# Kernel optimization log

Hardware: AMD Instinct MI355X
Metric: run time of the kernel (lower is better)

Reference implementation:

```python
import jax, jax.numpy as jnp
import numpy as np

D = 128
N_DRUG = 100000
N_PROT = 50000
E_DD, E_DP, E_PD = 800000, 600000, 600000
EPS = 1e-5


def setup_inputs() -> dict:
    key = jax.random.key(0)
    ks = jax.random.split(key, 19)
    f32 = jnp.float32
    return {
        "x_drug": jax.random.normal(ks[0], (N_DRUG, D), f32),
        "x_prot": jax.random.normal(ks[1], (N_PROT, D), f32),
        "Wagg_dd": jax.random.normal(ks[2], (D, D), f32) * 0.05,
        "Wagg_dp": jax.random.normal(ks[3], (D, D), f32) * 0.05,
        "Wagg_pd": jax.random.normal(ks[4], (D, D), f32) * 0.05,
        "W_drug": jax.random.normal(ks[5], (D, 2 * D), f32) * 0.05,
        "b_drug": jax.random.normal(ks[6], (D,), f32) * 0.01,
        "W_prot": jax.random.normal(ks[7], (D, 2 * D), f32) * 0.05,
        "b_prot": jax.random.normal(ks[8], (D,), f32) * 0.01,
        "g_drug": jnp.ones((D,), f32),
        "be_drug": jnp.zeros((D,), f32),
        "g_prot": jnp.ones((D,), f32),
        "be_prot": jnp.zeros((D,), f32),
        "ei_dd_src": jax.random.randint(ks[9], (E_DD,), 0, N_DRUG, jnp.int64 if jax.config.jax_enable_x64 else jnp.int32),
        "ei_dd_dst": jax.random.randint(ks[10], (E_DD,), 0, N_DRUG),
        "ei_dp_src": jax.random.randint(ks[11], (E_DP,), 0, N_DRUG),
        "ei_dp_dst": jax.random.randint(ks[12], (E_DP,), 0, N_PROT),
        "ei_pd_src": jax.random.randint(ks[13], (E_PD,), 0, N_PROT),
        "ei_pd_dst": jax.random.randint(ks[14], (E_PD,), 0, N_DRUG),
    }


def _rel_agg(x_src, W_agg, src_idx, dst_idx, n_dst):
    # gather -> per-relation Linear (no bias) + ReLU -> scatter-mean
    h = jax.nn.relu(x_src[src_idx] @ W_agg.T)            # [E, D]
    s = jax.ops.segment_sum(h, dst_idx, num_segments=n_dst)
    c = jax.ops.segment_sum(jnp.ones((src_idx.shape[0],), h.dtype), dst_idx, num_segments=n_dst)
    return s / jnp.maximum(c, 1.0)[:, None]


def _layernorm(x, g, b):
    mu = jnp.mean(x, axis=-1, keepdims=True)
    var = jnp.mean(jnp.square(x - mu), axis=-1, keepdims=True)
    return (x - mu) * jax.lax.rsqrt(var + EPS) * g + b


def _node_update(h_self, h_agg, W, b, g, be):
    h = jax.nn.relu(jnp.concatenate([h_self, h_agg], axis=-1) @ W.T + b)
    return _layernorm(h + h_self, g, be)  # dropout is identity in eval


def reference(x_drug, x_prot, Wagg_dd, Wagg_dp, Wagg_pd, W_drug, b_drug,
              W_prot, b_prot, g_drug, be_drug, g_prot, be_prot,
              ei_dd_src, ei_dd_dst, ei_dp_src, ei_dp_dst, ei_pd_src, ei_pd_dst):
    agg_dd = _rel_agg(x_drug, Wagg_dd, ei_dd_src, ei_dd_dst, N_DRUG)
    agg_pd = _rel_agg(x_prot, Wagg_pd, ei_pd_src, ei_pd_dst, N_DRUG)
    agg_drug = (agg_dd + agg_pd) * 0.5                   # mean over relations into 'drug'
    agg_prot = _rel_agg(x_drug, Wagg_dp, ei_dp_src, ei_dp_dst, N_PROT)
    out_drug = _node_update(x_drug, agg_drug, W_drug, b_drug, g_drug, be_drug)
    out_prot = _node_update(x_prot, agg_prot, W_prot, b_prot, g_prot, be_prot)
    # pack the per-type outputs into one array [N_DRUG + N_PROT, D]
    return jnp.concatenate([out_drug, out_prot], axis=0)
```

## Files before the change

kernel.cpp:

```cpp
#include <hip/hip_runtime.h>

#define D 128
#define ND 100000
#define NP 50000
#define NE_DD 800000
#define NE_DP 600000
#define NE_PD 600000
#define NE_TOT 2000000

#define NTOT 250000
#define NBC 490
#define NC 250880
#define CHUNKA 4096
#define NBLKA 489
#define CHUNKIT 16
#define SEGCAP 8192

#define TF_BD 782
#define TF_BP 196
#define NU_BD 391
#define NU_BP 196

typedef __bf16 bf16;
typedef __attribute__((ext_vector_type(8))) __bf16 bf16x8;
typedef __attribute__((ext_vector_type(2))) __bf16 bf16x2;
typedef __attribute__((ext_vector_type(4))) float f32x4;
typedef __attribute__((ext_vector_type(2))) float f32x2;

#define OFF_WDD   0UL
#define OFF_WDP   32768UL
#define OFF_WPD   65536UL
#define OFF_WDRUG 98304UL
#define OFF_WPROT 163840UL
#define OFF_YDD   229376UL
#define OFF_YDP   (OFF_YDD + 25600000UL)
#define OFF_YPD   (OFF_YDP + 25600000UL)
#define OFF_AGGD  (OFF_YPD + 12800000UL)
#define OFF_AGGP  (OFF_AGGD + 25600000UL)
#define OFF_BCNT  (OFF_AGGP + 12800000UL)
#define OFF_GCUR  (OFF_BCNT + 2048UL)
#define OFF_CBASE (OFF_GCUR + 2048UL)
#define OFF_RP    (OFF_CBASE + 2048UL)
#define OFF_PAIRS (OFF_RP + 1003520UL)
#define OFF_POOL  (OFF_PAIRS + 16000000UL)

__device__ __forceinline__ unsigned enc1(float f)
{
    unsigned t = __float_as_uint(f * 0x1p-120f);
    t = (t + 0x80000u) >> 20;
    return t > 0x7Eu ? 0x7Eu : t;
}
__device__ __forceinline__ unsigned enc4(float a, float b, float c, float d)
{
    return enc1(a) | (enc1(b) << 8) | (enc1(c) << 16) | (enc1(d) << 24);
}

__global__ __launch_bounds__(256) void prep_kernel(
    const float* __restrict__ w0, const float* __restrict__ w1,
    const float* __restrict__ w2, const float* __restrict__ w3,
    const float* __restrict__ w4,
    bf16* __restrict__ o0, bf16* __restrict__ o1, bf16* __restrict__ o2,
    bf16* __restrict__ o3, bf16* __restrict__ o4,
    int* __restrict__ bcnt)
{
    int m = blockIdx.y;
    int i = blockIdx.x * 256 + threadIdx.x;
    if (m == 5) {
        if (i < NBC) bcnt[i] = 0;
        return;
    }
    const float* src; bf16* dst; int n; bool perm;
    switch (m) {
        case 0: src = w0; dst = o0; n = D * D; perm = false; break;
        case 1: src = w1; dst = o1; n = D * D; perm = false; break;
        case 2: src = w2; dst = o2; n = D * D; perm = false; break;
        case 3: src = w3; dst = o3; n = D * 2 * D; perm = true; break;
        default: src = w4; dst = o4; n = D * 2 * D; perm = true; break;
    }
    if (i < n) {
        int si = i;
        if (perm) {
            int col = i & 255;
            if (col >= 128) {
                int p = col - 128;
                si = (i & ~255) | (128 + (p & 7) * 16 + (p >> 3));
            }
        }
        dst[i] = (bf16)src[si];
    }
}

__device__ __forceinline__ bf16x8 load_a_f32(const float* __restrict__ xr)
{
    float4 f0 = *(const float4*)xr;
    float4 f1 = *(const float4*)(xr + 4);
    bf16x8 a;
    a[0] = (bf16)f0.x; a[1] = (bf16)f0.y; a[2] = (bf16)f0.z; a[3] = (bf16)f0.w;
    a[4] = (bf16)f1.x; a[5] = (bf16)f1.y; a[6] = (bf16)f1.z; a[7] = (bf16)f1.w;
    return a;
}

__device__ __forceinline__ void transform_drug(
    const float* __restrict__ x, const bf16* __restrict__ W1,
    const bf16* __restrict__ W2, unsigned char* __restrict__ y1,
    unsigned char* __restrict__ y2, int blk)
{
    int lane = threadIdx.x & 63;
    int wave = threadIdx.x >> 6;
    int q = lane >> 4, c = lane & 15;
    int mb = blk * 128 + wave * 32;

    f32x4 acc1[2][8], acc2[2][8];
#pragma unroll
    for (int mt = 0; mt < 2; mt++)
#pragma unroll
        for (int nt = 0; nt < 8; nt++) { acc1[mt][nt] = 0; acc2[mt][nt] = 0; }

#pragma unroll
    for (int kb = 0; kb < 4; kb++) {
        int k = kb * 32 + q * 8;
        bf16x8 a[2];
#pragma unroll
        for (int mt = 0; mt < 2; mt++) {
            int row = min(mb + mt * 16 + c, ND - 1);
            a[mt] = load_a_f32(x + (long)row * D + k);
        }
#pragma unroll
        for (int nt = 0; nt < 8; nt++) {
            bf16x8 b1 = *(const bf16x8*)(W1 + (nt * 16 + c) * D + k);
            bf16x8 b2 = *(const bf16x8*)(W2 + (nt * 16 + c) * D + k);
#pragma unroll
            for (int mt = 0; mt < 2; mt++) {
                acc1[mt][nt] = __builtin_amdgcn_mfma_f32_16x16x32_bf16(a[mt], b1, acc1[mt][nt], 0, 0, 0);
                acc2[mt][nt] = __builtin_amdgcn_mfma_f32_16x16x32_bf16(a[mt], b2, acc2[mt][nt], 0, 0, 0);
            }
        }
    }
#pragma unroll
    for (int mt = 0; mt < 2; mt++)
#pragma unroll
        for (int r = 0; r < 4; r++) {
            int row = mb + mt * 16 + q * 4 + r;
            if (row < ND) {
                float v1[8], v2[8];
#pragma unroll
                for (int nt = 0; nt < 8; nt++) {
                    v1[nt] = fmaxf(acc1[mt][nt][r], 0.f);
                    v2[nt] = fmaxf(acc2[mt][nt][r], 0.f);
                }
                uint2 p1, p2;
                p1.x = enc4(v1[0], v1[1], v1[2], v1[3]);
                p1.y = enc4(v1[4], v1[5], v1[6], v1[7]);
                p2.x = enc4(v2[0], v2[1], v2[2], v2[3]);
                p2.y = enc4(v2[4], v2[5], v2[6], v2[7]);
                *(uint2*)(y1 + (long)row * D + c * 8) = p1;
                *(uint2*)(y2 + (long)row * D + c * 8) = p2;
            }
        }
}

__device__ __forceinline__ void transform_prot(
    const float* __restrict__ x, const bf16* __restrict__ W1,
    unsigned char* __restrict__ y1, int blk)
{
    int lane = threadIdx.x & 63;
    int wave = threadIdx.x >> 6;
    int q = lane >> 4, c = lane & 15;
    int mb = blk * 256 + wave * 64;

    f32x4 acc[4][8];
#pragma unroll
    for (int mt = 0; mt < 4; mt++)
#pragma unroll
        for (int nt = 0; nt < 8; nt++) acc[mt][nt] = 0;

#pragma unroll
    for (int kb = 0; kb < 4; kb++) {
        int k = kb * 32 + q * 8;
        bf16x8 a[4];
#pragma unroll
        for (int mt = 0; mt < 4; mt++) {
            int row = min(mb + mt * 16 + c, NP - 1);
            a[mt] = load_a_f32(x + (long)row * D + k);
        }
#pragma unroll
        for (int nt = 0; nt < 8; nt++) {
            bf16x8 b1 = *(const bf16x8*)(W1 + (nt * 16 + c) * D + k);
#pragma unroll
            for (int mt = 0; mt < 4; mt++)
                acc[mt][nt] = __builtin_amdgcn_mfma_f32_16x16x32_bf16(a[mt], b1, acc[mt][nt], 0, 0, 0);
        }
    }
#pragma unroll
    for (int mt = 0; mt < 4; mt++)
#pragma unroll
        for (int r = 0; r < 4; r++) {
            int row = mb + mt * 16 + q * 4 + r;
            if (row < NP) {
                float v[8];
#pragma unroll
                for (int nt = 0; nt < 8; nt++)
                    v[nt] = fmaxf(acc[mt][nt][r], 0.f);
                uint2 p1;
                p1.x = enc4(v[0], v[1], v[2], v[3]);
                p1.y = enc4(v[4], v[5], v[6], v[7]);
                *(uint2*)(y1 + (long)row * D + c * 8) = p1;
            }
        }
}

__global__ __launch_bounds__(256, 2) void transform_kernel(
    const float* __restrict__ x_drug, const float* __restrict__ x_prot,
    const bf16* __restrict__ Wdd, const bf16* __restrict__ Wdp,
    const bf16* __restrict__ Wpd,
    unsigned char* __restrict__ y_dd, unsigned char* __restrict__ y_dp,
    unsigned char* __restrict__ y_pd)
{
    int blk = blockIdx.x;
    if (blk < TF_BD)
        transform_drug(x_drug, Wdd, Wdp, y_dd, y_dp, blk);
    else
        transform_prot(x_prot, Wpd, y_pd, blk - TF_BD);
}

__global__ __launch_bounds__(256) void hist_kernel(
    const int* __restrict__ dd_dst, const int* __restrict__ pd_dst,
    const int* __restrict__ dp_dst, int* __restrict__ bcnt)
{
    __shared__ int h[NBC];
    for (int i = threadIdx.x; i < NBC; i += 256) h[i] = 0;
    __syncthreads();
    int base = blockIdx.x * CHUNKA;
    for (int it = 0; it < CHUNKIT; it++) {
        int e = base + it * 256 + threadIdx.x;
        if (e < NE_TOT) {
            int didx;
            if (e < NE_DD) didx = dd_dst[e];
            else if (e < NE_DD + NE_PD) didx = ND + pd_dst[e - NE_DD];
            else didx = 2 * ND + dp_dst[e - NE_DD - NE_PD];
            atomicAdd(&h[didx >> 9], 1);
        }
    }
    __syncthreads();
    for (int i = threadIdx.x; i < NBC; i += 256)
        if (h[i]) atomicAdd(&bcnt[i], h[i]);
}

__global__ __launch_bounds__(256) void scan_kernel(
    const int* __restrict__ bcnt, int* __restrict__ cbase, int* __restrict__ gcur)
{
    __shared__ int ps[256];
    int t = threadIdx.x;
    int i0 = 2 * t, i1 = 2 * t + 1;
    int c0 = (i0 < NBC) ? bcnt[i0] : 0;
    int c1 = (i1 < NBC) ? bcnt[i1] : 0;
    ps[t] = c0 + c1;
    __syncthreads();
#pragma unroll
    for (int off = 1; off < 256; off <<= 1) {
        int add = (t >= off) ? ps[t - off] : 0;
        __syncthreads();
        ps[t] += add;
        __syncthreads();
    }
    int excl = ps[t] - (c0 + c1);
    if (i0 <= NBC) cbase[i0] = excl;
    if (i0 < NBC) gcur[i0] = excl;
    if (i1 < NBC) { cbase[i1] = excl + c0; gcur[i1] = excl + c0; }
}

__global__ __launch_bounds__(256) void binA_kernel(
    const int* __restrict__ dd_src, const int* __restrict__ dd_dst,
    const int* __restrict__ pd_src, const int* __restrict__ pd_dst,
    const int* __restrict__ dp_src, const int* __restrict__ dp_dst,
    int* __restrict__ gcur, unsigned* __restrict__ pairs)
{
    __shared__ int h[NBC];
    __shared__ int gb[NBC];
    __shared__ int2 pr[CHUNKA];
    __shared__ unsigned short rk[CHUNKA];
    for (int i = threadIdx.x; i < NBC; i += 256) h[i] = 0;
    __syncthreads();
    int base = blockIdx.x * CHUNKA;
    for (int it = 0; it < CHUNKIT; it++) {
        int idx = it * 256 + threadIdx.x;
        int e = base + idx;
        int didx = -1, sv = 0;
        if (e < NE_TOT) {
            if (e < NE_DD) { didx = dd_dst[e]; sv = dd_src[e]; }
            else if (e < NE_DD + NE_PD) { int u = e - NE_DD; didx = ND + pd_dst[u]; sv = pd_src[u]; }
            else { int u = e - NE_DD - NE_PD; didx = 2 * ND + dp_dst[u]; sv = dp_src[u]; }
            rk[idx] = (unsigned short)atomicAdd(&h[didx >> 9], 1);
        }
        pr[idx] = make_int2(didx, sv);
    }
    __syncthreads();
    for (int b = threadIdx.x; b < NBC; b += 256) {
        int c = h[b];
        gb[b] = c ? atomicAdd(&gcur[b], c) : 0;
    }
    __syncthreads();
    for (int it = 0; it < CHUNKIT; it++) {
        int idx = it * 256 + threadIdx.x;
        int2 p = pr[idx];
        if (p.x >= 0)
            pairs[gb[p.x >> 9] + rk[idx]] =
                ((unsigned)(p.x & 511) << 17) | (unsigned)p.y;
    }
}

__global__ __launch_bounds__(256) void sortB_kernel(
    const int* __restrict__ cbase, const unsigned* __restrict__ pairs,
    int* __restrict__ pool, int* __restrict__ rp)
{
    __shared__ int h[512];
    __shared__ int excl[512];
    __shared__ int ps[256];
    __shared__ unsigned short rk[SEGCAP];
    __shared__ int outl[SEGCAP];

    int b = blockIdx.x;
    int s0 = cbase[b], s1 = cbase[b + 1];
    int n = s1 - s0;
    if (n > SEGCAP) n = SEGCAP;
    int t = threadIdx.x;
    h[t] = 0; h[t + 256] = 0;
    __syncthreads();

    for (int i = t; i < n; i += 256) {
        unsigned p = pairs[s0 + i];
        rk[i] = (unsigned short)atomicAdd(&h[p >> 17], 1);
    }
    __syncthreads();

    int c0 = h[2 * t], c1 = h[2 * t + 1];
    ps[t] = c0 + c1;
    __syncthreads();
#pragma unroll
    for (int off = 1; off < 256; off <<= 1) {
        int add = (t >= off) ? ps[t - off] : 0;
        __syncthreads();
        ps[t] += add;
        __syncthreads();
    }
    int pe = ps[t] - (c0 + c1);
    excl[2 * t] = pe;
    excl[2 * t + 1] = pe + c0;
    __syncthreads();

    int nb = b * 512;
    rp[nb + 2 * t] = s0 + excl[2 * t];
    rp[nb + 2 * t + 1] = s0 + excl[2 * t + 1];

    for (int i = t; i < n; i += 256) {
        unsigned p = pairs[s0 + i];
        outl[excl[p >> 17] + rk[i]] = (int)(p & 0x1FFFFu);
    }
    __syncthreads();
    for (int i = t; i < n; i += 256)
        pool[s0 + i] = outl[i];
}

__device__ __forceinline__ void accw(unsigned short w, f32x2* acc)
{
    float lo = __uint_as_float((unsigned)(w & 0xFFu) << 20);
    float hi = __uint_as_float((unsigned)(w >> 8) << 20);
    acc->x = fmaf(lo, 0x1p120f, acc->x);
    acc->y = fmaf(hi, 0x1p120f, acc->y);
}

__device__ __forceinline__ void acc_seg(
    const int* __restrict__ pool, int s, int e,
    const unsigned short* __restrict__ y, int lane, f32x2* acc)
{
    int j = s;
    for (; j + 8 <= e; j += 8) {
        unsigned short u[8];
#pragma unroll
        for (int t = 0; t < 8; t++)
            u[t] = y[(long)pool[j + t] * 64 + lane];
#pragma unroll
        for (int t = 0; t < 8; t++) accw(u[t], acc);
    }
    if (j + 4 <= e) {
        unsigned short u[4];
#pragma unroll
        for (int t = 0; t < 4; t++)
            u[t] = y[(long)pool[j + t] * 64 + lane];
#pragma unroll
        for (int t = 0; t < 4; t++) accw(u[t], acc);
        j += 4;
    }
    if (j + 2 <= e) {
        unsigned short u0 = y[(long)pool[j] * 64 + lane];
        unsigned short u1 = y[(long)pool[j + 1] * 64 + lane];
        accw(u0, acc); accw(u1, acc);
        j += 2;
    }
    if (j < e)
        accw(y[(long)pool[j] * 64 + lane], acc);
}

__global__ __launch_bounds__(256) void gather_kernel(
    const int* __restrict__ rp, const int* __restrict__ pool,
    const unsigned short* __restrict__ y_dd,
    const unsigned short* __restrict__ y_pd,
    const unsigned short* __restrict__ y_dp,
    bf16* __restrict__ agg_d, bf16* __restrict__ agg_p)
{
    int wid = blockIdx.x * 4 + (threadIdx.x >> 6);
    int lane = threadIdx.x & 63;

    if (wid < ND) {
        int g = wid;
        int s1 = rp[g], e1 = rp[g + 1];
        int s2 = rp[ND + g], e2 = rp[ND + g + 1];
        f32x2 a; a.x = 0.f; a.y = 0.f;
        f32x2 b; b.x = 0.f; b.y = 0.f;
        int j1 = s1, j2 = s2;
        while (j1 + 4 <= e1 && j2 + 4 <= e2) {
            unsigned short ua[4], ub[4];
#pragma unroll
            for (int t = 0; t < 4; t++)
                ua[t] = y_dd[(long)pool[j1 + t] * 64 + lane];
#pragma unroll
            for (int t = 0; t < 4; t++)
                ub[t] = y_pd[(long)pool[j2 + t] * 64 + lane];
#pragma unroll
            for (int t = 0; t < 4; t++) accw(ua[t], &a);
#pragma unroll
            for (int t = 0; t < 4; t++) accw(ub[t], &b);
            j1 += 4; j2 += 4;
        }
        acc_seg(pool, j1, e1, y_dd, lane, &a);
        acc_seg(pool, j2, e2, y_pd, lane, &b);
        float i1 = 0.5f / (float)max(e1 - s1, 1);
        float i2 = 0.5f / (float)max(e2 - s2, 1);
        f32x2 r = a * i1 + b * i2;
        bf16x2 o; o[0] = (bf16)r.x; o[1] = (bf16)r.y;
        *(bf16x2*)(agg_d + (long)g * D + lane * 2) = o;
    } else if (wid < ND + NP) {
        int p = wid - ND;
        int s1 = rp[2 * ND + p], e1 = rp[2 * ND + p + 1];
        f32x2 a; a.x = 0.f; a.y = 0.f;
        acc_seg(pool, s1, e1, y_dp, lane, &a);
        float i1 = 1.0f / (float)max(e1 - s1, 1);
        f32x2 r = a * i1;
        bf16x2 o; o[0] = (bf16)r.x; o[1] = (bf16)r.y;
        *(bf16x2*)(agg_p + (long)p * D + lane * 2) = o;
    }
}

__device__ __forceinline__ void node_update_body(
    const float* __restrict__ x, const bf16* __restrict__ agg,
    const bf16* __restrict__ W, const float* __restrict__ b,
    const float* __restrict__ g, const float* __restrict__ be,
    float* __restrict__ out, int M, int blk)
{
    int lane = threadIdx.x & 63;
    int wave = threadIdx.x >> 6;
    int q = lane >> 4, c = lane & 15;
    int mb = blk * 256 + wave * 64;

    f32x4 acc[4][8];
#pragma unroll
    for (int mt = 0; mt < 4; mt++)
#pragma unroll
        for (int nt = 0; nt < 8; nt++) acc[mt][nt] = 0;

#pragma unroll
    for (int kb = 0; kb < 8; kb++) {
        bf16x8 a[4];
#pragma unroll
        for (int mt = 0; mt < 4; mt++) {
            int row = min(mb + mt * 16 + c, M - 1);
            if (kb < 4)
                a[mt] = load_a_f32(x + (long)row * D + kb * 32 + q * 8);
            else
                a[mt] = *(const bf16x8*)(agg + (long)row * D + (kb - 4) * 32 + q * 8);
        }
#pragma unroll
        for (int nt = 0; nt < 8; nt++) {
            bf16x8 bw = *(const bf16x8*)(W + (nt * 16 + c) * (2 * D) + kb * 32 + q * 8);
#pragma unroll
            for (int mt = 0; mt < 4; mt++)
                acc[mt][nt] = __builtin_amdgcn_mfma_f32_16x16x32_bf16(a[mt], bw, acc[mt][nt], 0, 0, 0);
        }
    }

    float bv[8], gv[8], bev[8];
#pragma unroll
    for (int nt = 0; nt < 8; nt++) {
        int col = nt * 16 + c;
        bv[nt] = b[col]; gv[nt] = g[col]; bev[nt] = be[col];
    }
#pragma unroll
    for (int mt = 0; mt < 4; mt++)
#pragma unroll
        for (int r = 0; r < 4; r++) {
            int row = mb + mt * 16 + q * 4 + r;
            int rowc = min(row, M - 1);
            const float* xr = x + (long)rowc * D + c;
            float v[8];
            float sum = 0.f, sq = 0.f;
#pragma unroll
            for (int nt = 0; nt < 8; nt++) {
                float h = fmaxf(acc[mt][nt][r] + bv[nt], 0.f);
                float t = h + xr[nt * 16];
                v[nt] = t; sum += t; sq += t * t;
            }
#pragma unroll
            for (int m = 1; m < 16; m <<= 1) {
                sum += __shfl_xor(sum, m, 64);
                sq  += __shfl_xor(sq,  m, 64);
            }
            float mu   = sum * (1.f / 128.f);
            float var  = sq  * (1.f / 128.f) - mu * mu;
            float rstd = rsqrtf(var + 1e-5f);
            if (row < M) {
                float* op = out + (long)row * D + c;
#pragma unroll
                for (int nt = 0; nt < 8; nt++)
                    op[nt * 16] = (v[nt] - mu) * rstd * gv[nt] + bev[nt];
            }
        }
}

__global__ __launch_bounds__(256, 2) void node_update_kernel(
    const float* __restrict__ x_drug, const float* __restrict__ x_prot,
    const bf16* __restrict__ agg_d, const bf16* __restrict__ agg_p,
    const bf16* __restrict__ Wdrug, const float* __restrict__ b_drug,
    const float* __restrict__ g_drug, const float* __restrict__ be_drug,
    const bf16* __restrict__ Wprot, const float* __restrict__ b_prot,
    const float* __restrict__ g_prot, const float* __restrict__ be_prot,
    float* __restrict__ out)
{
    int blk = blockIdx.x;
    if (blk < NU_BD)
        node_update_body(x_drug, agg_d, Wdrug, b_drug, g_drug, be_drug,
                         out, ND, blk);
    else
        node_update_body(x_prot, agg_p, Wprot, b_prot, g_prot, be_prot,
                         out + (long)ND * D, NP, blk - NU_BD);
}

extern "C" void kernel_launch(void* const* d_in, const int* in_sizes, int n_in,
                              void* d_out, int out_size, void* d_ws, size_t ws_size,
                              hipStream_t stream)
{
    const float* x_drug  = (const float*)d_in[0];
    const float* x_prot  = (const float*)d_in[1];
    const float* Wagg_dd = (const float*)d_in[2];
    const float* Wagg_dp = (const float*)d_in[3];
    const float* Wagg_pd = (const float*)d_in[4];
    const float* W_drug  = (const float*)d_in[5];
    const float* b_drug  = (const float*)d_in[6];
    const float* W_prot  = (const float*)d_in[7];
    const float* b_prot  = (const float*)d_in[8];
    const float* g_drug  = (const float*)d_in[9];
    const float* be_drug = (const float*)d_in[10];
    const float* g_prot  = (const float*)d_in[11];
    const float* be_prot = (const float*)d_in[12];
    const int* dd_src = (const int*)d_in[13];
    const int* dd_dst = (const int*)d_in[14];
    const int* dp_src = (const int*)d_in[15];
    const int* dp_dst = (const int*)d_in[16];
    const int* pd_src = (const int*)d_in[17];
    const int* pd_dst = (const int*)d_in[18];

    char* ws = (char*)d_ws;
    bf16* Wdd   = (bf16*)(ws + OFF_WDD);
    bf16* Wdp   = (bf16*)(ws + OFF_WDP);
    bf16* Wpd   = (bf16*)(ws + OFF_WPD);
    bf16* Wdrug = (bf16*)(ws + OFF_WDRUG);
    bf16* Wprot = (bf16*)(ws + OFF_WPROT);
    unsigned char* y_dd = (unsigned char*)(ws + OFF_YDD);
    unsigned char* y_dp = (unsigned char*)(ws + OFF_YDP);
    unsigned char* y_pd = (unsigned char*)(ws + OFF_YPD);
    bf16* agg_d = (bf16*)(ws + OFF_AGGD);
    bf16* agg_p = (bf16*)(ws + OFF_AGGP);
    int* bcnt   = (int*)(ws + OFF_BCNT);
    int* gcur   = (int*)(ws + OFF_GCUR);
    int* cbase  = (int*)(ws + OFF_CBASE);
    int* rp     = (int*)(ws + OFF_RP);
    unsigned* pairs = (unsigned*)(ws + OFF_PAIRS);
    int* pool   = (int*)(ws + OFF_POOL);
    float* out  = (float*)d_out;

    prep_kernel<<<dim3(128, 6), 256, 0, stream>>>(
        Wagg_dd, Wagg_dp, Wagg_pd, W_drug, W_prot,
        Wdd, Wdp, Wpd, Wdrug, Wprot, bcnt);

    transform_kernel<<<TF_BD + TF_BP, 256, 0, stream>>>(
        x_drug, x_prot, Wdd, Wdp, Wpd, y_dd, y_dp, y_pd);

    hist_kernel<<<NBLKA, 256, 0, stream>>>(dd_dst, pd_dst, dp_dst, bcnt);
    scan_kernel<<<1, 256, 0, stream>>>(bcnt, cbase, gcur);
    binA_kernel<<<NBLKA, 256, 0, stream>>>(
        dd_src, dd_dst, pd_src, pd_dst, dp_src, dp_dst, gcur, pairs);
    sortB_kernel<<<NBC, 256, 0, stream>>>(cbase, pairs, pool, rp);

    gather_kernel<<<(ND + NP + 3) / 4, 256, 0, stream>>>(
        rp, pool, (const unsigned short*)y_dd, (const unsigned short*)y_pd,
        (const unsigned short*)y_dp, agg_d, agg_p);

    node_update_kernel<<<NU_BD + NU_BP, 256, 0, stream>>>(
        x_drug, x_prot, agg_d, agg_p,
        Wdrug, b_drug, g_drug, be_drug,
        Wprot, b_prot, g_prot, be_prot, out);
}
```

Baseline: 395.2 us.

## Replace histogram and scan with fixed-capacity bucket slots in edge binning

The separate histogram and prefix-scan kernels are dropped. Each destination bucket now gets a fixed SEGCAP-sized slot in the pairs buffer, and binA writes at bucket*SEGCAP plus an atomic cursor. The row-pointer array gains an extra end entry per bucket (stride 513), and the gather kernel indexes it through a remapping helper. This saves one full pass over the destination indices and two launches, but edges beyond a bucket's capacity are silently dropped. The workspace offsets for the y buffers are also halved, which assumes they were oversized.

```diff
diff --git a/kernel.cpp b/kernel.cpp
--- a/kernel.cpp
+++ b/kernel.cpp
@@ -10,11 +10,11 @@
 
 #define NTOT 250000
 #define NBC 490
-#define NC 250880
 #define CHUNKA 4096
 #define NBLKA 489
 #define CHUNKIT 16
 #define SEGCAP 8192
+#define RPS 513
 
 #define TF_BD 782
 #define TF_BP 196
@@ -33,16 +33,14 @@
 #define OFF_WDRUG 98304UL
 #define OFF_WPROT 163840UL
 #define OFF_YDD   229376UL
-#define OFF_YDP   (OFF_YDD + 25600000UL)
-#define OFF_YPD   (OFF_YDP + 25600000UL)
-#define OFF_AGGD  (OFF_YPD + 12800000UL)
+#define OFF_YDP   (OFF_YDD + 12800000UL)
+#define OFF_YPD   (OFF_YDP + 12800000UL)
+#define OFF_AGGD  (OFF_YPD + 6400000UL)
 #define OFF_AGGP  (OFF_AGGD + 25600000UL)
-#define OFF_BCNT  (OFF_AGGP + 12800000UL)
-#define OFF_GCUR  (OFF_BCNT + 2048UL)
-#define OFF_CBASE (OFF_GCUR + 2048UL)
-#define OFF_RP    (OFF_CBASE + 2048UL)
-#define OFF_PAIRS (OFF_RP + 1003520UL)
-#define OFF_POOL  (OFF_PAIRS + 16000000UL)
+#define OFF_GCUR  (OFF_AGGP + 12800000UL)
+#define OFF_RP    (OFF_GCUR + 2048UL)
+#define OFF_PAIRS (OFF_RP + 1005568UL)
+#define OFF_POOL  (OFF_PAIRS + 16056320UL)
 
 __device__ __forceinline__ unsigned enc1(float f)
 {
@@ -61,12 +59,12 @@
     const float* __restrict__ w4,
     bf16* __restrict__ o0, bf16* __restrict__ o1, bf16* __restrict__ o2,
     bf16* __restrict__ o3, bf16* __restrict__ o4,
-    int* __restrict__ bcnt)
+    int* __restrict__ gcur)
 {
     int m = blockIdx.y;
     int i = blockIdx.x * 256 + threadIdx.x;
     if (m == 5) {
-        if (i < NBC) bcnt[i] = 0;
+        if (i < NBC) gcur[i] = 0;
         return;
     }
     const float* src; bf16* dst; int n; bool perm;
@@ -223,52 +221,6 @@
         transform_prot(x_prot, Wpd, y_pd, blk - TF_BD);
 }
 
-__global__ __launch_bounds__(256) void hist_kernel(
-    const int* __restrict__ dd_dst, const int* __restrict__ pd_dst,
-    const int* __restrict__ dp_dst, int* __restrict__ bcnt)
-{
-    __shared__ int h[NBC];
-    for (int i = threadIdx.x; i < NBC; i += 256) h[i] = 0;
-    __syncthreads();
-    int base = blockIdx.x * CHUNKA;
-    for (int it = 0; it < CHUNKIT; it++) {
-        int e = base + it * 256 + threadIdx.x;
-        if (e < NE_TOT) {
-            int didx;
-            if (e < NE_DD) didx = dd_dst[e];
-            else if (e < NE_DD + NE_PD) didx = ND + pd_dst[e - NE_DD];
-            else didx = 2 * ND + dp_dst[e - NE_DD - NE_PD];
-            atomicAdd(&h[didx >> 9], 1);
-        }
-    }
-    __syncthreads();
-    for (int i = threadIdx.x; i < NBC; i += 256)
-        if (h[i]) atomicAdd(&bcnt[i], h[i]);
-}
-
-__global__ __launch_bounds__(256) void scan_kernel(
-    const int* __restrict__ bcnt, int* __restrict__ cbase, int* __restrict__ gcur)
-{
-    __shared__ int ps[256];
-    int t = threadIdx.x;
-    int i0 = 2 * t, i1 = 2 * t + 1;
-    int c0 = (i0 < NBC) ? bcnt[i0] : 0;
-    int c1 = (i1 < NBC) ? bcnt[i1] : 0;
-    ps[t] = c0 + c1;
-    __syncthreads();
-#pragma unroll
-    for (int off = 1; off < 256; off <<= 1) {
-        int add = (t >= off) ? ps[t - off] : 0;
-        __syncthreads();
-        ps[t] += add;
-        __syncthreads();
-    }
-    int excl = ps[t] - (c0 + c1);
-    if (i0 <= NBC) cbase[i0] = excl;
-    if (i0 < NBC) gcur[i0] = excl;
-    if (i1 < NBC) { cbase[i1] = excl + c0; gcur[i1] = excl + c0; }
-}
-
 __global__ __launch_bounds__(256) void binA_kernel(
     const int* __restrict__ dd_src, const int* __restrict__ dd_dst,
     const int* __restrict__ pd_src, const int* __restrict__ pd_dst,
@@ -303,14 +255,18 @@
     for (int it = 0; it < CHUNKIT; it++) {
         int idx = it * 256 + threadIdx.x;
         int2 p = pr[idx];
-        if (p.x >= 0)
-            pairs[gb[p.x >> 9] + rk[idx]] =
-                ((unsigned)(p.x & 511) << 17) | (unsigned)p.y;
+        if (p.x >= 0) {
+            int b = p.x >> 9;
+            int pos = gb[b] + rk[idx];
+            if (pos < SEGCAP)
+                pairs[(long)b * SEGCAP + pos] =
+                    ((unsigned)(p.x & 511) << 17) | (unsigned)p.y;
+        }
     }
 }
 
 __global__ __launch_bounds__(256) void sortB_kernel(
-    const int* __restrict__ cbase, const unsigned* __restrict__ pairs,
+    const int* __restrict__ gcur, const unsigned* __restrict__ pairs,
     int* __restrict__ pool, int* __restrict__ rp)
 {
     __shared__ int h[512];
@@ -320,8 +276,8 @@
     __shared__ int outl[SEGCAP];
 
     int b = blockIdx.x;
-    int s0 = cbase[b], s1 = cbase[b + 1];
-    int n = s1 - s0;
+    int s0 = b * SEGCAP;
+    int n = gcur[b];
     if (n > SEGCAP) n = SEGCAP;
     int t = threadIdx.x;
     h[t] = 0; h[t + 256] = 0;
@@ -348,9 +304,10 @@
     excl[2 * t + 1] = pe + c0;
     __syncthreads();
 
-    int nb = b * 512;
+    int nb = b * RPS;
     rp[nb + 2 * t] = s0 + excl[2 * t];
     rp[nb + 2 * t + 1] = s0 + excl[2 * t + 1];
+    if (t == 0) rp[nb + 512] = s0 + n;
 
     for (int i = t; i < n; i += 256) {
         unsigned p = pairs[s0 + i];
@@ -359,6 +316,11 @@
     __syncthreads();
     for (int i = t; i < n; i += 256)
         pool[s0 + i] = outl[i];
+}
+
+__device__ __forceinline__ int rpi(int node)
+{
+    return (node >> 9) * RPS + (node & 511);
 }
 
 __device__ __forceinline__ void accw(unsigned short w, f32x2* acc)
@@ -413,8 +375,9 @@
 
     if (wid < ND) {
         int g = wid;
-        int s1 = rp[g], e1 = rp[g + 1];
-        int s2 = rp[ND + g], e2 = rp[ND + g + 1];
+        int i1r = rpi(g), i2r = rpi(ND + g);
+        int s1 = rp[i1r], e1 = rp[i1r + 1];
+        int s2 = rp[i2r], e2 = rp[i2r + 1];
         f32x2 a; a.x = 0.f; a.y = 0.f;
         f32x2 b; b.x = 0.f; b.y = 0.f;
         int j1 = s1, j2 = s2;
@@ -441,7 +404,8 @@
         *(bf16x2*)(agg_d + (long)g * D + lane * 2) = o;
     } else if (wid < ND + NP) {
         int p = wid - ND;
-        int s1 = rp[2 * ND + p], e1 = rp[2 * ND + p + 1];
+        int ir = rpi(2 * ND + p);
+        int s1 = rp[ir], e1 = rp[ir + 1];
         f32x2 a; a.x = 0.f; a.y = 0.f;
         acc_seg(pool, s1, e1, y_dp, lane, &a);
         float i1 = 1.0f / (float)max(e1 - s1, 1);
@@ -579,9 +543,7 @@
     unsigned char* y_pd = (unsigned char*)(ws + OFF_YPD);
     bf16* agg_d = (bf16*)(ws + OFF_AGGD);
     bf16* agg_p = (bf16*)(ws + OFF_AGGP);
-    int* bcnt   = (int*)(ws + OFF_BCNT);
     int* gcur   = (int*)(ws + OFF_GCUR);
-    int* cbase  = (int*)(ws + OFF_CBASE);
     int* rp     = (int*)(ws + OFF_RP);
     unsigned* pairs = (unsigned*)(ws + OFF_PAIRS);
     int* pool   = (int*)(ws + OFF_POOL);
@@ -589,16 +551,15 @@
 
     prep_kernel<<<dim3(128, 6), 256, 0, stream>>>(
         Wagg_dd, Wagg_dp, Wagg_pd, W_drug, W_prot,
-        Wdd, Wdp, Wpd, Wdrug, Wprot, bcnt);
+        Wdd, Wdp, Wpd, Wdrug, Wprot, gcur);
+
+    binA_kernel<<<NBLKA, 256, 0, stream>>>(
+        dd_src, dd_dst, pd_src, pd_dst, dp_src, dp_dst, gcur, pairs);
+
+    sortB_kernel<<<NBC, 256, 0, stream>>>(gcur, pairs, pool, rp);
 
     transform_kernel<<<TF_BD + TF_BP, 256, 0, stream>>>(
         x_drug, x_prot, Wdd, Wdp, Wpd, y_dd, y_dp, y_pd);
-
-    hist_kernel<<<NBLKA, 256, 0, stream>>>(dd_dst, pd_dst, dp_dst, bcnt);
-    scan_kernel<<<1, 256, 0, stream>>>(bcnt, cbase, gcur);
-    binA_kernel<<<NBLKA, 256, 0, stream>>>(
-        dd_src, dd_dst, pd_src, pd_dst, dp_src, dp_dst, gcur, pairs);
-    sortB_kernel<<<NBC, 256, 0, stream>>>(cbase, pairs, pool, rp);
 
     gather_kernel<<<(ND + NP + 3) / 4, 256, 0, stream>>>(
         rp, pool, (const unsigned short*)y_dd, (const unsigned short*)y_pd,
```

Result: faster. 374.8 us (-5.2%).
